# Optimization experiments

Hardware: AMD Instinct MI355X
Metric: run time of the kernel (lower is better)

## Reference

```python
import jax, jax.numpy as jnp
import numpy as np

B, T, N, F = 16, 12, 30000, 4
K = 3                       # receptive_field
ORDER = 1 + 2 * K           # bidirectional -> 7
HID = 128
OUT_CH = HID - HID % ORDER  # 126
GOUT = OUT_CH // ORDER      # 18 (grouped conv1d, kernel_size=1)
MLP_H = 64
HOR, OUT = 12, 4
EMB = 32
E = 960_000


def setup_inputs() -> dict:
    key = jax.random.key(0)
    ks = jax.random.split(key, 12)
    return dict(
        x=jax.random.normal(ks[0], (B, T, N, F), jnp.float32),
        edge_index=jax.random.randint(ks[1], (2, E), 0, N),
        edge_weight=jax.random.uniform(ks[2], (E,), jnp.float32),
        conv_w=jax.random.normal(ks[3], (ORDER, F, GOUT), jnp.float32) * 0.1,
        conv_b=jnp.zeros((OUT_CH,), jnp.float32),
        node_emb=jax.random.normal(ks[4], (N, EMB), jnp.float32) * 0.1,
        emb_w=jax.random.normal(ks[5], (EMB, OUT_CH), jnp.float32) * 0.1,
        emb_b=jnp.zeros((OUT_CH,), jnp.float32),
        mlp_w=jax.random.normal(ks[6], (OUT_CH, MLP_H), jnp.float32) * 0.1,
        mlp_b=jnp.zeros((MLP_H,), jnp.float32),
        ro_w=jax.random.normal(ks[7], (MLP_H, HOR * OUT), jnp.float32) * 0.1,
        ro_b=jnp.zeros((HOR * OUT,), jnp.float32),
    )


def _norm_w(w, agg_idx, n):
    # random-walk normalization at the aggregation node
    deg = jax.ops.segment_sum(w, agg_idx, num_segments=n)
    return w / jnp.maximum(deg[agg_idx], 1e-8)


def _khop(x, src, dst, wn, k):
    # k hops of gather(src) -> scale -> scatter-add(dst); x: [B,N,F]
    outs = []
    cur = x
    for _ in range(k):
        msgs = cur[:, src, :] * wn[None, :, None]          # [B,E,F]
        cur = jnp.zeros_like(cur).at[:, dst, :].add(msgs)  # [B,N,F]
        outs.append(cur)
    return outs


def reference(x, edge_weight, conv_w, conv_b, node_emb, emb_w, emb_b,
              mlp_w, mlp_b, ro_w, ro_b, edge_index):
    xt = x[:, -1]                       # [B,N,F] last time step
    src, dst = edge_index[0], edge_index[1]
    n = xt.shape[1]

    # SGP spatial embedding: [x, A x..A^k x, A^T x..(A^T)^k x]
    wn_fwd = _norm_w(edge_weight, dst, n)
    wn_bwd = _norm_w(edge_weight, src, n)
    hops = [xt] + _khop(xt, src, dst, wn_fwd, K) + _khop(xt, dst, src, wn_bwd, K)
    h = jnp.stack(hops, axis=2)         # [B,N,ORDER,F] == concat order of cat(...,-1)

    # grouped Conv1d (kernel=1, groups=ORDER): per-hop linear F -> GOUT
    h = jnp.einsum('bngi,gio->bngo', h, conv_w).reshape(B, n, OUT_CH) + conv_b
    h = jax.nn.silu(h)

    # positional (node) embedding
    h = h + (node_emb @ emb_w + emb_b)[None]

    # MLP (1 dense layer) + linear readout over horizon
    h = jax.nn.silu(h @ mlp_w + mlp_b)                 # [B,N,MLP_H]
    y = h @ ro_w + ro_b                                # [B,N,HOR*OUT]
    return y.reshape(B, n, HOR, OUT).transpose(0, 2, 1, 3)  # [B,HOR,N,OUT]
```

## Files before the change

kernel.cpp:

```cpp
#include <hip/hip_runtime.h>
#include <hip/hip_bf16.h>

#define NB 16
#define NT 12
#define NN 30000
#define NF 4
#define NE 960000
#define ORDER 7
#define GOUT 18
#define OUT_CH 126
#define MLP_H 64
#define HOR 12
#define NOUT 4
#define EMB 32
#define CAP 96
#define NREP 8

typedef unsigned short u16;
typedef __attribute__((ext_vector_type(8))) _Float16 f16x8;
typedef __attribute__((ext_vector_type(4))) float f32x4;
typedef __attribute__((ext_vector_type(4))) int i32x4;

__device__ __forceinline__ float silu_f(float x) {
    return x * __builtin_amdgcn_rcpf(1.0f + __expf(-x));
}

__device__ __forceinline__ u16 f2h(float x) {
    union { _Float16 h; u16 u; } cv;
    cv.h = (_Float16)x;
    return cv.u;
}

__device__ __forceinline__ float h2f(u16 u) {
    union { u16 u2; _Float16 h; } c; c.u2 = u;
    return (float)c.h;
}

__device__ __forceinline__ float2 h2f2(unsigned v) {
    union { unsigned u; _Float16 h[2]; } c; c.u = v;
    return make_float2((float)c.h[0], (float)c.h[1]);
}

__device__ __forceinline__ unsigned packh2(float x, float y) {
    union { u16 h[2]; unsigned u; } c;
    c.h[0] = f2h(x); c.h[1] = f2h(y);
    return c.u;
}

__device__ __forceinline__ int xcc_id() {
    int x;
    asm("s_getreg_b32 %0, hwreg(HW_REG_XCC_ID)" : "=s"(x));
    return x & 7;
}

#define WSCALE (1.0f / 65535.0f)

#define CNT8_BLKS 469
#define SC_BLKS 938
#define TR_BLKS 1875
#define NPG_BLKS 469


__global__ __launch_bounds__(256) void k_cnt(
    const int* __restrict__ ei,
    int* cntRF, int* cntRB, unsigned* __restrict__ rnk)
{
    int rep = xcc_id();
    int* cF = cntRF + rep * NN;
    int* cB = cntRB + rep * NN;
    int e0 = blockIdx.x * 2048 + threadIdx.x * 8;
    if (e0 + 8 > NE) return;
    int4 sa = *(const int4*)&ei[e0];
    int4 sb = *(const int4*)&ei[e0 + 4];
    int4 da = *(const int4*)&ei[NE + e0];
    int4 db = *(const int4*)&ei[NE + e0 + 4];
    int ss[8] = {sa.x, sa.y, sa.z, sa.w, sb.x, sb.y, sb.z, sb.w};
    int dd[8] = {da.x, da.y, da.z, da.w, db.x, db.y, db.z, db.w};
    int2 r[8];
    int one = 1;
    #pragma unroll
    for (int k = 0; k < 8; ++k) {
        asm volatile("global_atomic_add %0, %1, %2, off sc0"
                     : "=&v"(r[k].x) : "v"(&cF[dd[k]]), "v"(one) : "memory");
        asm volatile("global_atomic_add %0, %1, %2, off sc0"
                     : "=&v"(r[k].y) : "v"(&cB[ss[k]]), "v"(one) : "memory");
    }
    __builtin_amdgcn_sched_barrier(0);
    asm volatile("s_waitcnt vmcnt(0)"
                 : "+v"(r[0].x), "+v"(r[0].y), "+v"(r[1].x), "+v"(r[1].y),
                   "+v"(r[2].x), "+v"(r[2].y), "+v"(r[3].x), "+v"(r[3].y),
                   "+v"(r[4].x), "+v"(r[4].y), "+v"(r[5].x), "+v"(r[5].y),
                   "+v"(r[6].x), "+v"(r[6].y), "+v"(r[7].x), "+v"(r[7].y)
                 :: "memory");
    __builtin_amdgcn_sched_barrier(0);
    unsigned repHi = (unsigned)rep << 16;
    uint4 p0, p1;
    p0.x = (unsigned)(r[0].x & 0xFF) | ((unsigned)(r[0].y & 0xFF) << 8) | repHi;
    p0.y = (unsigned)(r[1].x & 0xFF) | ((unsigned)(r[1].y & 0xFF) << 8) | repHi;
    p0.z = (unsigned)(r[2].x & 0xFF) | ((unsigned)(r[2].y & 0xFF) << 8) | repHi;
    p0.w = (unsigned)(r[3].x & 0xFF) | ((unsigned)(r[3].y & 0xFF) << 8) | repHi;
    p1.x = (unsigned)(r[4].x & 0xFF) | ((unsigned)(r[4].y & 0xFF) << 8) | repHi;
    p1.y = (unsigned)(r[5].x & 0xFF) | ((unsigned)(r[5].y & 0xFF) << 8) | repHi;
    p1.z = (unsigned)(r[6].x & 0xFF) | ((unsigned)(r[6].y & 0xFF) << 8) | repHi;
    p1.w = (unsigned)(r[7].x & 0xFF) | ((unsigned)(r[7].y & 0xFF) << 8) | repHi;
    *(uint4*)&rnk[e0]     = p0;
    *(uint4*)&rnk[e0 + 4] = p1;
}


__global__ __launch_bounds__(256) void k_misc(
    const float* __restrict__ x,
    const float* __restrict__ mlp_w, const float* __restrict__ ro_w,
    const float* __restrict__ conv_w, const float* __restrict__ emb_w,
    u16* __restrict__ WmG, u16* __restrict__ RoG, u16* __restrict__ CwB,
    u16* __restrict__ EwB, u16* __restrict__ xtH)
{
    int bid = blockIdx.x;
    int t = threadIdx.x;
    if (bid == 0) {
        int j = t & 63, kb0 = t >> 6;
        #pragma unroll
        for (int kk = 0; kk < 4; ++kk) {
            int kch = kb0 + kk * 4;
            int c0 = kch * 8;
            unsigned wd[4];
            #pragma unroll
            for (int p = 0; p < 4; ++p) {
                float va = (c0 + 2*p     < 126) ? mlp_w[(c0 + 2*p    ) * 64 + j] : 0.f;
                float vb = (c0 + 2*p + 1 < 126) ? mlp_w[(c0 + 2*p + 1) * 64 + j] : 0.f;
                wd[p] = (unsigned)f2h(va) | ((unsigned)f2h(vb) << 16);
            }
            *(uint4*)&WmG[(kch * 64 + j) * 8] = make_uint4(wd[0], wd[1], wd[2], wd[3]);
        }
    } else if (bid == 1) {
        #pragma unroll
        for (int kk = 0; kk < 2; ++kk) {
            int i = t + kk * 256;
            if (i < 384) {
                int kch = i / 48, o = i - kch * 48;
                int k0 = kch * 8;
                unsigned wd[4];
                #pragma unroll
                for (int p = 0; p < 4; ++p)
                    wd[p] = (unsigned)f2h(ro_w[(k0 + 2*p) * 48 + o])
                          | ((unsigned)f2h(ro_w[(k0 + 2*p + 1) * 48 + o]) << 16);
                *(uint4*)&RoG[(kch * 48 + o) * 8] = make_uint4(wd[0], wd[1], wd[2], wd[3]);
            }
        }
    } else if (bid == 2) {
        #pragma unroll
        for (int j = 0; j < 16; ++j) {
            int idx = t + j * 256;
            int kch = idx >> 10, rem = idx & 1023, n = rem >> 3, e = rem & 7;
            int k = kch * 8 + e;
            float val = 0.f;
            if (k < 28 && n < 126) {
                int g = k >> 2, i = k & 3, q = n - g * 18;
                if (q >= 0 && q < 18) val = conv_w[(g * 4 + i) * 18 + q];
            }
            CwB[idx] = f2h(val);
        }
    } else if (bid == 3) {
        #pragma unroll
        for (int j = 0; j < 16; ++j) {
            int idx = t + j * 256;
            int kch = idx >> 10, rem = idx & 1023, n = rem >> 3, e = rem & 7;
            int k = kch * 8 + e;
            float val = (n < 126) ? emb_w[k * 126 + n] : 0.f;
            EwB[idx] = f2h(val);
        }
    } else {
        int idx = (bid - 4) * 256 + t;
        int b = idx / NN;
        int n = idx - b * NN;
        float4 v = *(const float4*)&x[((((size_t)b * NT) + (NT - 1)) * NN + n) * NF];
        uint2 p;
        p.x = packh2(v.x, v.y);
        p.y = packh2(v.z, v.w);
        *(uint2*)&xtH[n * 64 + b * 4] = p;
    }
}


__global__ __launch_bounds__(256) void k_npg(
    const float* __restrict__ nemb, const float* __restrict__ emb_b,
    const u16* __restrict__ EwB, u16* __restrict__ npG)
{
    __shared__ __align__(16) u16 A_lds[64 * 32];
    __shared__ float ebL[128];
    const int t = threadIdx.x;
    const int n0 = blockIdx.x * 64;
    {
        int ks = t >> 6, r = t & 63;
        int n = n0 + r;
        float4 va = make_float4(0.f, 0.f, 0.f, 0.f), vb = va;
        if (n < NN) {
            va = *(const float4*)&nemb[(size_t)n * 32 + ks * 8];
            vb = *(const float4*)&nemb[(size_t)n * 32 + ks * 8 + 4];
        }
        uint4 p;
        p.x = packh2(va.x, va.y);
        p.y = packh2(va.z, va.w);
        p.z = packh2(vb.x, vb.y);
        p.w = packh2(vb.z, vb.w);
        *(uint4*)&A_lds[(ks * 64 + r) * 8] = p;
    }
    if (t < 128) ebL[t] = (t < 126) ? emb_b[t] : 0.f;
    __syncthreads();

    const int lane = t & 63, w = t >> 6;
    const int lg = lane >> 4, lm = lane & 15;
    f32x4 acc[8];
    #pragma unroll
    for (int nc = 0; nc < 8; ++nc) {
        float eb = ebL[nc * 16 + lm];
        acc[nc][0] = eb; acc[nc][1] = eb; acc[nc][2] = eb; acc[nc][3] = eb;
    }
    f16x8 a = *(const f16x8*)&A_lds[(lg * 64 + w * 16 + lm) * 8];
    #pragma unroll
    for (int nc = 0; nc < 8; ++nc) {
        f16x8 b = *(const f16x8*)&EwB[(lg * 128 + nc * 16 + lm) * 8];
        acc[nc] = __builtin_amdgcn_mfma_f32_16x16x32_f16(a, b, acc[nc], 0, 0, 0);
    }
    #pragma unroll
    for (int nc = 0; nc < 8; ++nc) {
        int col = nc * 16 + lm;
        #pragma unroll
        for (int reg = 0; reg < 4; ++reg) {
            int row = w * 16 + lg * 4 + reg;
            int n = n0 + row;
            if (n < NN) npG[(size_t)n * 128 + col] = f2h(acc[nc][reg]);
        }
    }
}


__global__ __launch_bounds__(256) void k_nodeprep(
    int* __restrict__ cntRF, int* __restrict__ cntRB,
    int* __restrict__ cntAF, int* __restrict__ cntAB)
{
    int i = blockIdx.x * 256 + threadIdx.x;
    if (i >= NN) return;
    int* cntR = (blockIdx.y == 0) ? cntRF : cntRB;
    int* cntA = (blockIdx.y == 0) ? cntAF : cntAB;
    int c = 0;
    #pragma unroll
    for (int r = 0; r < NREP; ++r) {
        int v = cntR[r * NN + i];
        cntR[r * NN + i] = c;
        c += v;
    }
    cntA[i] = c;
}


__global__ __launch_bounds__(256) void k_scatter(
    const int* __restrict__ ei, const float* __restrict__ ew,
    const int* __restrict__ cntRF, const int* __restrict__ cntRB,
    const unsigned* __restrict__ rnk,
    unsigned* __restrict__ csrF, unsigned* __restrict__ csrB)
{
    int e0 = blockIdx.x * 1024 + threadIdx.x * 4;
    if (e0 >= NE) return;
    if (e0 + 4 <= NE) {
        int4 s4 = *(const int4*)&ei[e0];
        int4 d4 = *(const int4*)&ei[NE + e0];
        float4 w4 = *(const float4*)&ew[e0];
        uint4 rp = *(const uint4*)&rnk[e0];
        unsigned rr[4] = {rp.x, rp.y, rp.z, rp.w};
        int ss[4] = {s4.x, s4.y, s4.z, s4.w};
        int dd[4] = {d4.x, d4.y, d4.z, d4.w};
        float wv[4] = {w4.x, w4.y, w4.z, w4.w};
        #pragma unroll
        for (int k = 0; k < 4; ++k) {
            unsigned wfix = (unsigned)(wv[k] * 65535.0f + 0.5f);
            int rep = rr[k] >> 16;
            int sF = cntRF[rep * NN + dd[k]] + (int)(rr[k] & 0xFF);
            int sB = cntRB[rep * NN + ss[k]] + (int)((rr[k] >> 8) & 0xFF);
            if (sF < CAP) csrF[(size_t)dd[k] * CAP + sF] = (unsigned)ss[k] | (wfix << 16);
            if (sB < CAP) csrB[(size_t)ss[k] * CAP + sB] = (unsigned)dd[k] | (wfix << 16);
        }
    } else {
        for (int k = 0; k < 4; ++k) {
            int e = e0 + k;
            if (e >= NE) break;
            int s = ei[e], d = ei[NE + e];
            unsigned wfix = (unsigned)(ew[e] * 65535.0f + 0.5f);
            unsigned r = rnk[e];
            int rep = r >> 16;
            int sF = cntRF[rep * NN + d] + (int)(r & 0xFF);
            int sB = cntRB[rep * NN + s] + (int)((r >> 8) & 0xFF);
            if (sF < CAP) csrF[(size_t)d * CAP + sF] = (unsigned)s | (wfix << 16);
            if (sB < CAP) csrB[(size_t)s * CAP + sB] = (unsigned)d | (wfix << 16);
        }
    }
}


__global__ __launch_bounds__(256) void k_hop(
    const u16* __restrict__ inF, u16* __restrict__ outF,
    const unsigned* __restrict__ csrF, const int* __restrict__ cntF,
    const u16* __restrict__ inB, u16* __restrict__ outB,
    const unsigned* __restrict__ csrB, const int* __restrict__ cntB)
{
    int lane = threadIdx.x & 63;
    int half = lane >> 5, l5 = lane & 31;
    int node = blockIdx.x * 4 + (threadIdx.x >> 6);
    if (node >= NN) return;
    const u16* in; u16* out; const unsigned* cs; const int* cntA;
    if (blockIdx.y == 0) { in = inF; out = outF; cs = csrF; cntA = cntF; }
    else                 { in = inB; out = outB; cs = csrB; cntA = cntB; }
    const unsigned* in4 = (const unsigned*)in;
    int cnt = min(cntA[node], CAP);
    const unsigned* seg = cs + (size_t)node * CAP;
    int full = cnt & ~7;
    float ax0 = 0.f, ay0 = 0.f, ax1 = 0.f, ay1 = 0.f;
    float ax2 = 0.f, ay2 = 0.f, ax3 = 0.f, ay3 = 0.f;
    float ws = 0.f;
    for (int j = 0; j < full; j += 8) {
        i32x4 q = __builtin_nontemporal_load((const i32x4*)&seg[j + 4 * half]);
        unsigned e0 = (unsigned)q.x, e1 = (unsigned)q.y;
        unsigned e2 = (unsigned)q.z, e3 = (unsigned)q.w;
        unsigned v0 = in4[(e0 & 0xFFFF) * 32 + l5];
        unsigned v1 = in4[(e1 & 0xFFFF) * 32 + l5];
        unsigned v2 = in4[(e2 & 0xFFFF) * 32 + l5];
        unsigned v3 = in4[(e3 & 0xFFFF) * 32 + l5];
        float w0 = (float)(e0 >> 16) * WSCALE;
        float w1 = (float)(e1 >> 16) * WSCALE;
        float w2 = (float)(e2 >> 16) * WSCALE;
        float w3 = (float)(e3 >> 16) * WSCALE;
        float2 f0 = h2f2(v0), f1 = h2f2(v1), f2 = h2f2(v2), f3 = h2f2(v3);
        ax0 += w0 * f0.x; ay0 += w0 * f0.y;
        ax1 += w1 * f1.x; ay1 += w1 * f1.y;
        ax2 += w2 * f2.x; ay2 += w2 * f2.y;
        ax3 += w3 * f3.x; ay3 += w3 * f3.y;
        ws += (w0 + w1) + (w2 + w3);
    }
    if (cnt & 7) {
        i32x4 q = *(const i32x4*)&seg[full + 4 * half];
        int b0 = full + 4 * half;
        unsigned e0 = (unsigned)q.x, e1 = (unsigned)q.y;
        unsigned e2 = (unsigned)q.z, e3 = (unsigned)q.w;
        unsigned m0 = (b0     < cnt) ? e0 : 0u;
        unsigned m1 = (b0 + 1 < cnt) ? e1 : 0u;
        unsigned m2 = (b0 + 2 < cnt) ? e2 : 0u;
        unsigned m3 = (b0 + 3 < cnt) ? e3 : 0u;
        unsigned v0 = in4[(m0 & 0xFFFF) * 32 + l5];
        unsigned v1 = in4[(m1 & 0xFFFF) * 32 + l5];
        unsigned v2 = in4[(m2 & 0xFFFF) * 32 + l5];
        unsigned v3 = in4[(m3 & 0xFFFF) * 32 + l5];
        float w0 = (float)(m0 >> 16) * WSCALE;
        float w1 = (float)(m1 >> 16) * WSCALE;
        float w2 = (float)(m2 >> 16) * WSCALE;
        float w3 = (float)(m3 >> 16) * WSCALE;
        float2 f0 = h2f2(v0), f1 = h2f2(v1), f2 = h2f2(v2), f3 = h2f2(v3);
        ax0 += w0 * f0.x; ay0 += w0 * f0.y;
        ax1 += w1 * f1.x; ay1 += w1 * f1.y;
        ax2 += w2 * f2.x; ay2 += w2 * f2.y;
        ax3 += w3 * f3.x; ay3 += w3 * f3.y;
        ws += (w0 + w1) + (w2 + w3);
    }
    float tx = (ax0 + ax1) + (ax2 + ax3);
    float ty = (ay0 + ay1) + (ay2 + ay3);
    tx += __shfl_xor(tx, 32);
    ty += __shfl_xor(ty, 32);
    ws += __shfl_xor(ws, 32);
    if (half == 0) {
        float inv = 1.0f / fmaxf(ws, 1e-8f);
        ((unsigned*)out)[node * 32 + l5] = packh2(tx * inv, ty * inv);
    }
}


__global__ __launch_bounds__(256) void k_fused(
    const u16* __restrict__ xtH,
    const u16* __restrict__ h1, const u16* __restrict__ h2,
    const u16* __restrict__ h3, const u16* __restrict__ h4,
    const u16* __restrict__ h5, const u16* __restrict__ h6,
    const u16* __restrict__ WmG, const u16* __restrict__ RoG,
    const u16* __restrict__ CwB, const u16* __restrict__ npG,
    const float* __restrict__ conv_b,
    const float* __restrict__ mlp_b, const float* __restrict__ ro_b,
    float* __restrict__ out)
{
    __shared__ __align__(16) u16 HtB[8192];
    __shared__ __align__(16) u16 C1B[4096];
    __shared__ __align__(16) float npL[512];
    __shared__ float cbL[128];
    __shared__ float mbL[64];
    __shared__ float rbL[48];

    u16* A_lds = C1B;

    const int t = threadIdx.x;
    const int n0 = blockIdx.x * 4;
    const int lane = t & 63;
    const int w = t >> 6;
    const int lg = lane >> 4, lm = lane & 15;

    {
        int ks = t >> 6, r = t & 63;
        uint2 a, b;
        if (ks == 0) {
            a = *(const uint2*)&xtH[n0 * 64 + r * 4];
            b = *(const uint2*)&h1[n0 * 64 + r * 4];
        } else if (ks == 1) {
            a = *(const uint2*)&h2[n0 * 64 + r * 4];
            b = *(const uint2*)&h3[n0 * 64 + r * 4];
        } else if (ks == 2) {
            a = *(const uint2*)&h4[n0 * 64 + r * 4];
            b = *(const uint2*)&h5[n0 * 64 + r * 4];
        } else {
            a = *(const uint2*)&h6[n0 * 64 + r * 4];
            b = make_uint2(0u, 0u);
        }
        *(uint4*)&A_lds[(ks * 64 + r) * 8] = make_uint4(a.x, a.y, b.x, b.y);
    }
    if (t < 128) cbL[t] = (t < 126) ? conv_b[t] : 0.f;
    if (t < 64) mbL[t] = mlp_b[t];
    if (t < 48) rbL[t] = ro_b[t];
    #pragma unroll
    for (int kk = 0; kk < 2; ++kk) {
        int i = t + kk * 256;
        npL[i] = h2f(npG[n0 * 128 + i]);
    }
    __syncthreads();

    {
        f32x4 acc[8];
        #pragma unroll
        for (int nc = 0; nc < 8; ++nc) {
            float cb = cbL[nc * 16 + lm];
            acc[nc][0] = cb; acc[nc][1] = cb; acc[nc][2] = cb; acc[nc][3] = cb;
        }
        f16x8 a = *(const f16x8*)&A_lds[(lg * 64 + w * 16 + lm) * 8];
        #pragma unroll
        for (int nc = 0; nc < 8; ++nc) {
            f16x8 b = *(const f16x8*)&CwB[(lg * 128 + nc * 16 + lm) * 8];
            acc[nc] = __builtin_amdgcn_mfma_f32_16x16x32_f16(a, b, acc[nc], 0, 0, 0);
        }
        #pragma unroll
        for (int nc = 0; nc < 8; ++nc) {
            int col = nc * 16 + lm;
            float npv = npL[w * 128 + col];
            #pragma unroll
            for (int reg = 0; reg < 4; ++reg) {
                int row = w * 16 + lg * 4 + reg;
                float val = silu_f(acc[nc][reg]) + npv;
                HtB[((col >> 3) * 64 + row) * 8 + (col & 7)] = f2h(val);
            }
        }
    }
    __syncthreads();

    {
        const int wr = w >> 1, wc = w & 1;
        float mb0 = mbL[wc * 32 + lm];
        float mb1 = mbL[wc * 32 + 16 + lm];
        f32x4 acc00 = {mb0, mb0, mb0, mb0};
        f32x4 acc01 = {mb1, mb1, mb1, mb1};
        f32x4 acc10 = {mb0, mb0, mb0, mb0};
        f32x4 acc11 = {mb1, mb1, mb1, mb1};
        #pragma unroll
        for (int kc = 0; kc < 4; ++kc) {
            const int kb = (kc * 4 + lg) * 64;
            f16x8 a0 = *(const f16x8*)&HtB[(kb + wr * 32 + lm) * 8];
            f16x8 a1 = *(const f16x8*)&HtB[(kb + wr * 32 + 16 + lm) * 8];
            f16x8 b0 = *(const f16x8*)&WmG[(kb + wc * 32 + lm) * 8];
            f16x8 b1 = *(const f16x8*)&WmG[(kb + wc * 32 + 16 + lm) * 8];
            acc00 = __builtin_amdgcn_mfma_f32_16x16x32_f16(a0, b0, acc00, 0, 0, 0);
            acc01 = __builtin_amdgcn_mfma_f32_16x16x32_f16(a0, b1, acc01, 0, 0, 0);
            acc10 = __builtin_amdgcn_mfma_f32_16x16x32_f16(a1, b0, acc10, 0, 0, 0);
            acc11 = __builtin_amdgcn_mfma_f32_16x16x32_f16(a1, b1, acc11, 0, 0, 0);
        }
        #pragma unroll
        for (int reg = 0; reg < 4; ++reg) {
            int row0 = wr * 32 + lg * 4 + reg;
            int col0 = wc * 32 + lm;
            C1B[((col0 >> 3) * 64 + row0) * 8 + (col0 & 7)] = f2h(silu_f(acc00[reg]));
            int col1 = col0 + 16;
            C1B[((col1 >> 3) * 64 + row0) * 8 + (col1 & 7)] = f2h(silu_f(acc01[reg]));
            int row1 = row0 + 16;
            C1B[((col0 >> 3) * 64 + row1) * 8 + (col0 & 7)] = f2h(silu_f(acc10[reg]));
            C1B[((col1 >> 3) * 64 + row1) * 8 + (col1 & 7)] = f2h(silu_f(acc11[reg]));
        }
    }
    __syncthreads();

    {
        const int rt3 = w * 16;
        float r0 = rbL[lm], r1 = rbL[16 + lm], r2 = rbL[32 + lm];
        f32x4 c0 = {r0, r0, r0, r0};
        f32x4 c1 = {r1, r1, r1, r1};
        f32x4 c2 = {r2, r2, r2, r2};
        #pragma unroll
        for (int kc = 0; kc < 2; ++kc) {
            const int kb = kc * 4 + lg;
            f16x8 a  = *(const f16x8*)&C1B[(kb * 64 + rt3 + lm) * 8];
            f16x8 b0 = *(const f16x8*)&RoG[(kb * 48 + lm) * 8];
            f16x8 b1 = *(const f16x8*)&RoG[(kb * 48 + 16 + lm) * 8];
            f16x8 b2 = *(const f16x8*)&RoG[(kb * 48 + 32 + lm) * 8];
            c0 = __builtin_amdgcn_mfma_f32_16x16x32_f16(a, b0, c0, 0, 0, 0);
            c1 = __builtin_amdgcn_mfma_f32_16x16x32_f16(a, b1, c1, 0, 0, 0);
            c2 = __builtin_amdgcn_mfma_f32_16x16x32_f16(a, b2, c2, 0, 0, 0);
        }
        float* C2L = (float*)HtB;
        #pragma unroll
        for (int reg = 0; reg < 4; ++reg) {
            int row = rt3 + lg * 4 + reg;
            C2L[row * 52 + lm]      = c0[reg];
            C2L[row * 52 + 16 + lm] = c1[reg];
            C2L[row * 52 + 32 + lm] = c2[reg];
        }
    }
    __syncthreads();

    if (t < 192) {
        int b = t / 12, hor = t - b * 12;
        const float* C2L = (const float*)HtB;
        #pragma unroll
        for (int nl2 = 0; nl2 < 4; ++nl2) {
            f32x4 v = *(const f32x4*)&C2L[(nl2 * 16 + b) * 52 + hor * 4];
            *(f32x4*)&out[(((size_t)b * 12 + hor) * 30000 + n0 + nl2) * 4] = v;
        }
    }
}


extern "C" void kernel_launch(void* const* d_in, const int* in_sizes, int n_in,
                              void* d_out, int out_size, void* d_ws, size_t ws_size,
                              hipStream_t stream)
{
    const float* x      = (const float*)d_in[0];
    const int*   ei     = (const int*)d_in[1];
    const float* ew     = (const float*)d_in[2];
    const float* conv_w = (const float*)d_in[3];
    const float* conv_b = (const float*)d_in[4];
    const float* nemb   = (const float*)d_in[5];
    const float* emb_w  = (const float*)d_in[6];
    const float* emb_b  = (const float*)d_in[7];
    const float* mlp_w  = (const float*)d_in[8];
    const float* mlp_b  = (const float*)d_in[9];
    const float* ro_w   = (const float*)d_in[10];
    const float* ro_b   = (const float*)d_in[11];
    float* out = (float*)d_out;

    char* ws = (char*)d_ws;
    size_t off = 0;
    auto alloc = [&](size_t bytes) -> char* {
        char* p = ws + off;
        off += (bytes + 255) & ~(size_t)255;
        return p;
    };

    int* cntRF  = (int*)alloc((size_t)NREP * NN * 4);
    int* cntRB  = (int*)alloc((size_t)NREP * NN * 4);
    size_t zeroBytes = off;

    int* cntAF  = (int*)alloc(NN * 4);
    int* cntAB  = (int*)alloc(NN * 4);
    unsigned* rnk = (unsigned*)alloc((size_t)NE * 4);
    unsigned* csrF = (unsigned*)alloc((size_t)NN * CAP * 4);
    unsigned* csrB = (unsigned*)alloc((size_t)NN * CAP * 4);
    u16* xtH    = (u16*)alloc((size_t)NN * 64 * 2);
    u16* hbuf[6];
    for (int i = 0; i < 6; ++i) hbuf[i] = (u16*)alloc((size_t)NN * 64 * 2);
    u16* npG    = (u16*)alloc((size_t)NN * 128 * 2);
    u16* WmG    = (u16*)alloc(8192 * 2);
    u16* RoG    = (u16*)alloc(3072 * 2);
    u16* CwB    = (u16*)alloc(4096 * 2);
    u16* EwB    = (u16*)alloc(4096 * 2);

    hipMemsetAsync(d_ws, 0, zeroBytes, stream);

    k_cnt<<<CNT8_BLKS, 256, 0, stream>>>(ei, cntRF, cntRB, rnk);
    k_misc<<<4 + TR_BLKS, 256, 0, stream>>>(
        x, mlp_w, ro_w, conv_w, emb_w,
        WmG, RoG, CwB, EwB, xtH);
    k_npg<<<NPG_BLKS, 256, 0, stream>>>(nemb, emb_b, EwB, npG);
    k_nodeprep<<<dim3((NN + 255) / 256, 2), 256, 0, stream>>>(
        cntRF, cntRB, cntAF, cntAB);
    k_scatter<<<SC_BLKS, 256, 0, stream>>>(ei, ew, cntRF, cntRB, rnk, csrF, csrB);

    dim3 nodeGrid((NN + 3) / 4, 2);
    k_hop<<<nodeGrid, 256, 0, stream>>>(xtH, hbuf[0], csrF, cntAF,
                                        xtH, hbuf[3], csrB, cntAB);
    k_hop<<<nodeGrid, 256, 0, stream>>>(hbuf[0], hbuf[1], csrF, cntAF,
                                        hbuf[3], hbuf[4], csrB, cntAB);
    k_hop<<<nodeGrid, 256, 0, stream>>>(hbuf[1], hbuf[2], csrF, cntAF,
                                        hbuf[4], hbuf[5], csrB, cntAB);

    k_fused<<<NN / 4, 256, 0, stream>>>(xtH, hbuf[0], hbuf[1], hbuf[2],
                                        hbuf[3], hbuf[4], hbuf[5],
                                        WmG, RoG, CwB, npG,
                                        conv_b, mlp_b, ro_b, out);
}
```

Baseline: 325.7 us.

## Replace global atomic degree counting with per-chunk LDS histograms

```diff
diff --git a/kernel.cpp b/kernel.cpp
--- a/kernel.cpp
+++ b/kernel.cpp
@@ -14,9 +14,12 @@
 #define NOUT 4
 #define EMB 32
 #define CAP 96
-#define NREP 8
+#define NCHUNK 64
+#define CHUNK 15000
+#define NHALF 15000
 
 typedef unsigned short u16;
+typedef unsigned char u8;
 typedef __attribute__((ext_vector_type(8))) _Float16 f16x8;
 typedef __attribute__((ext_vector_type(4))) float f32x4;
 typedef __attribute__((ext_vector_type(4))) int i32x4;
@@ -47,15 +50,8 @@
     return c.u;
 }
 
-__device__ __forceinline__ int xcc_id() {
-    int x;
-    asm("s_getreg_b32 %0, hwreg(HW_REG_XCC_ID)" : "=s"(x));
-    return x & 7;
-}
-
 #define WSCALE (1.0f / 65535.0f)
 
-#define CNT8_BLKS 469
 #define SC_BLKS 938
 #define TR_BLKS 1875
 #define NPG_BLKS 469
@@ -63,48 +59,28 @@
 
 __global__ __launch_bounds__(256) void k_cnt(
     const int* __restrict__ ei,
-    int* cntRF, int* cntRB, unsigned* __restrict__ rnk)
-{
-    int rep = xcc_id();
-    int* cF = cntRF + rep * NN;
-    int* cB = cntRB + rep * NN;
-    int e0 = blockIdx.x * 2048 + threadIdx.x * 8;
-    if (e0 + 8 > NE) return;
-    int4 sa = *(const int4*)&ei[e0];
-    int4 sb = *(const int4*)&ei[e0 + 4];
-    int4 da = *(const int4*)&ei[NE + e0];
-    int4 db = *(const int4*)&ei[NE + e0 + 4];
-    int ss[8] = {sa.x, sa.y, sa.z, sa.w, sb.x, sb.y, sb.z, sb.w};
-    int dd[8] = {da.x, da.y, da.z, da.w, db.x, db.y, db.z, db.w};
-    int2 r[8];
-    int one = 1;
-    #pragma unroll
-    for (int k = 0; k < 8; ++k) {
-        asm volatile("global_atomic_add %0, %1, %2, off sc0"
-                     : "=&v"(r[k].x) : "v"(&cF[dd[k]]), "v"(one) : "memory");
-        asm volatile("global_atomic_add %0, %1, %2, off sc0"
-                     : "=&v"(r[k].y) : "v"(&cB[ss[k]]), "v"(one) : "memory");
-    }
-    __builtin_amdgcn_sched_barrier(0);
-    asm volatile("s_waitcnt vmcnt(0)"
-                 : "+v"(r[0].x), "+v"(r[0].y), "+v"(r[1].x), "+v"(r[1].y),
-                   "+v"(r[2].x), "+v"(r[2].y), "+v"(r[3].x), "+v"(r[3].y),
-                   "+v"(r[4].x), "+v"(r[4].y), "+v"(r[5].x), "+v"(r[5].y),
-                   "+v"(r[6].x), "+v"(r[6].y), "+v"(r[7].x), "+v"(r[7].y)
-                 :: "memory");
-    __builtin_amdgcn_sched_barrier(0);
-    unsigned repHi = (unsigned)rep << 16;
-    uint4 p0, p1;
-    p0.x = (unsigned)(r[0].x & 0xFF) | ((unsigned)(r[0].y & 0xFF) << 8) | repHi;
-    p0.y = (unsigned)(r[1].x & 0xFF) | ((unsigned)(r[1].y & 0xFF) << 8) | repHi;
-    p0.z = (unsigned)(r[2].x & 0xFF) | ((unsigned)(r[2].y & 0xFF) << 8) | repHi;
-    p0.w = (unsigned)(r[3].x & 0xFF) | ((unsigned)(r[3].y & 0xFF) << 8) | repHi;
-    p1.x = (unsigned)(r[4].x & 0xFF) | ((unsigned)(r[4].y & 0xFF) << 8) | repHi;
-    p1.y = (unsigned)(r[5].x & 0xFF) | ((unsigned)(r[5].y & 0xFF) << 8) | repHi;
-    p1.z = (unsigned)(r[6].x & 0xFF) | ((unsigned)(r[6].y & 0xFF) << 8) | repHi;
-    p1.w = (unsigned)(r[7].x & 0xFF) | ((unsigned)(r[7].y & 0xFF) << 8) | repHi;
-    *(uint4*)&rnk[e0]     = p0;
-    *(uint4*)&rnk[e0 + 4] = p1;
+    int* __restrict__ cntRF, int* __restrict__ cntRB,
+    u8* __restrict__ rnkF, u8* __restrict__ rnkB)
+{
+    __shared__ int hist[NHALF];
+    int t = threadIdx.x;
+    int chunk = blockIdx.x, half = blockIdx.y, dir = blockIdx.z;
+    const int* nodes = (dir == 0) ? (ei + NE) : ei;
+    u8* rnk = (dir == 0) ? rnkF : rnkB;
+    int* cntOut = ((dir == 0) ? cntRF : cntRB) + chunk * NN + half * NHALF;
+    int base = half * NHALF;
+    for (int i = t; i < NHALF; i += 256) hist[i] = 0;
+    __syncthreads();
+    int e0 = chunk * CHUNK;
+    for (int i = t; i < CHUNK; i += 256) {
+        int n = nodes[e0 + i] - base;
+        if ((unsigned)n < (unsigned)NHALF) {
+            int r = atomicAdd(&hist[n], 1);
+            rnk[e0 + i] = (u8)r;
+        }
+    }
+    __syncthreads();
+    for (int i = t; i < NHALF; i += 256) cntOut[i] = hist[i];
 }
 
 
@@ -244,8 +220,8 @@
     int* cntR = (blockIdx.y == 0) ? cntRF : cntRB;
     int* cntA = (blockIdx.y == 0) ? cntAF : cntAB;
     int c = 0;
-    #pragma unroll
-    for (int r = 0; r < NREP; ++r) {
+    #pragma unroll 8
+    for (int r = 0; r < NCHUNK; ++r) {
         int v = cntR[r * NN + i];
         cntR[r * NN + i] = c;
         c += v;
@@ -257,26 +233,30 @@
 __global__ __launch_bounds__(256) void k_scatter(
     const int* __restrict__ ei, const float* __restrict__ ew,
     const int* __restrict__ cntRF, const int* __restrict__ cntRB,
-    const unsigned* __restrict__ rnk,
+    const u8* __restrict__ rnkF, const u8* __restrict__ rnkB,
     unsigned* __restrict__ csrF, unsigned* __restrict__ csrB)
 {
     int e0 = blockIdx.x * 1024 + threadIdx.x * 4;
     if (e0 >= NE) return;
+    int rep = e0 / CHUNK;
+    const int* pF = cntRF + rep * NN;
+    const int* pB = cntRB + rep * NN;
     if (e0 + 4 <= NE) {
         int4 s4 = *(const int4*)&ei[e0];
         int4 d4 = *(const int4*)&ei[NE + e0];
         float4 w4 = *(const float4*)&ew[e0];
-        uint4 rp = *(const uint4*)&rnk[e0];
-        unsigned rr[4] = {rp.x, rp.y, rp.z, rp.w};
+        uchar4 rf = *(const uchar4*)&rnkF[e0];
+        uchar4 rb = *(const uchar4*)&rnkB[e0];
+        int rfv[4] = {rf.x, rf.y, rf.z, rf.w};
+        int rbv[4] = {rb.x, rb.y, rb.z, rb.w};
         int ss[4] = {s4.x, s4.y, s4.z, s4.w};
         int dd[4] = {d4.x, d4.y, d4.z, d4.w};
         float wv[4] = {w4.x, w4.y, w4.z, w4.w};
         #pragma unroll
         for (int k = 0; k < 4; ++k) {
             unsigned wfix = (unsigned)(wv[k] * 65535.0f + 0.5f);
-            int rep = rr[k] >> 16;
-            int sF = cntRF[rep * NN + dd[k]] + (int)(rr[k] & 0xFF);
-            int sB = cntRB[rep * NN + ss[k]] + (int)((rr[k] >> 8) & 0xFF);
+            int sF = pF[dd[k]] + rfv[k];
+            int sB = pB[ss[k]] + rbv[k];
             if (sF < CAP) csrF[(size_t)dd[k] * CAP + sF] = (unsigned)ss[k] | (wfix << 16);
             if (sB < CAP) csrB[(size_t)ss[k] * CAP + sB] = (unsigned)dd[k] | (wfix << 16);
         }
@@ -286,10 +266,8 @@
             if (e >= NE) break;
             int s = ei[e], d = ei[NE + e];
             unsigned wfix = (unsigned)(ew[e] * 65535.0f + 0.5f);
-            unsigned r = rnk[e];
-            int rep = r >> 16;
-            int sF = cntRF[rep * NN + d] + (int)(r & 0xFF);
-            int sB = cntRB[rep * NN + s] + (int)((r >> 8) & 0xFF);
+            int sF = pF[d] + (int)rnkF[e];
+            int sB = pB[s] + (int)rnkB[e];
             if (sF < CAP) csrF[(size_t)d * CAP + sF] = (unsigned)s | (wfix << 16);
             if (sB < CAP) csrB[(size_t)s * CAP + sB] = (unsigned)d | (wfix << 16);
         }
@@ -553,13 +531,12 @@
         return p;
     };
 
-    int* cntRF  = (int*)alloc((size_t)NREP * NN * 4);
-    int* cntRB  = (int*)alloc((size_t)NREP * NN * 4);
-    size_t zeroBytes = off;
-
+    int* cntRF  = (int*)alloc((size_t)NCHUNK * NN * 4);
+    int* cntRB  = (int*)alloc((size_t)NCHUNK * NN * 4);
     int* cntAF  = (int*)alloc(NN * 4);
     int* cntAB  = (int*)alloc(NN * 4);
-    unsigned* rnk = (unsigned*)alloc((size_t)NE * 4);
+    u8* rnkF    = (u8*)alloc(NE);
+    u8* rnkB    = (u8*)alloc(NE);
     unsigned* csrF = (unsigned*)alloc((size_t)NN * CAP * 4);
     unsigned* csrB = (unsigned*)alloc((size_t)NN * CAP * 4);
     u16* xtH    = (u16*)alloc((size_t)NN * 64 * 2);
@@ -571,16 +548,16 @@
     u16* CwB    = (u16*)alloc(4096 * 2);
     u16* EwB    = (u16*)alloc(4096 * 2);
 
-    hipMemsetAsync(d_ws, 0, zeroBytes, stream);
-
-    k_cnt<<<CNT8_BLKS, 256, 0, stream>>>(ei, cntRF, cntRB, rnk);
+
+    k_cnt<<<dim3(NCHUNK, 2, 2), 256, 0, stream>>>(ei, cntRF, cntRB, rnkF, rnkB);
     k_misc<<<4 + TR_BLKS, 256, 0, stream>>>(
         x, mlp_w, ro_w, conv_w, emb_w,
         WmG, RoG, CwB, EwB, xtH);
     k_npg<<<NPG_BLKS, 256, 0, stream>>>(nemb, emb_b, EwB, npG);
     k_nodeprep<<<dim3((NN + 255) / 256, 2), 256, 0, stream>>>(
         cntRF, cntRB, cntAF, cntAB);
-    k_scatter<<<SC_BLKS, 256, 0, stream>>>(ei, ew, cntRF, cntRB, rnk, csrF, csrB);
+    k_scatter<<<SC_BLKS, 256, 0, stream>>>(ei, ew, cntRF, cntRB,
+                                           rnkF, rnkB, csrF, csrB);
 
     dim3 nodeGrid((NN + 3) / 4, 2);
     k_hop<<<nodeGrid, 256, 0, stream>>>(xtH, hbuf[0], csrF, cntAF,
```

Result: faster. 290.8 us (-10.7%).
